# Kernel optimization log

Measured on AMD Instinct MI355X. Metric: run time of the kernel, lower is better.

The kernel has to match this reference:

```python
import jax, jax.numpy as jnp
from jax import lax
import numpy as np

HID = 64      # lstm hidden / gat in-dim
HEADS = 4
DH = HID // HEADS  # 16 per-head dim
OUT = 3       # horizon


def setup_inputs() -> dict:
    key = jax.random.key(0)
    ks = jax.random.split(key, 18)
    B, T, N = 8, 12, 1500
    p = lambda k, shape: jax.random.normal(k, shape, jnp.float32) * 0.1
    return {
        "x": jax.random.normal(ks[0], (B, T, N), jnp.float32),
        "adj": jax.random.randint(ks[1], (N, N), 0, 2, jnp.int32),
        "lstm_Wih0": p(ks[2], (4 * HID, 1)),
        "lstm_Whh0": p(ks[3], (4 * HID, HID)),
        "lstm_bih0": p(ks[4], (4 * HID,)),
        "lstm_bhh0": p(ks[5], (4 * HID,)),
        "lstm_Wih1": p(ks[6], (4 * HID, HID)),
        "lstm_Whh1": p(ks[7], (4 * HID, HID)),
        "lstm_bih1": p(ks[8], (4 * HID,)),
        "lstm_bhh1": p(ks[9], (4 * HID,)),
        "gat0_W": p(ks[10], (HID, HID)),
        "gat0_asrc": p(ks[11], (HEADS, DH)),
        "gat0_adst": p(ks[12], (HEADS, DH)),
        "gat1_W": p(ks[13], (HID, HID)),
        "gat1_asrc": p(ks[14], (HEADS, DH)),
        "gat1_adst": p(ks[15], (HEADS, DH)),
        "out_W": p(ks[16], (OUT, HID)),
        "out_b": p(ks[17], (OUT,)),
    }


def _lstm_layer(seq, Wih, Whh, bih, bhh):
    # seq: (T, BN, in) -> (T, BN, H). PyTorch gate order i,f,g,o.
    BN = seq.shape[1]
    H = Whh.shape[1]

    def step(carry, xt):
        h, c = carry
        g = xt @ Wih.T + h @ Whh.T + bih + bhh
        i, f, gg, o = jnp.split(g, 4, axis=-1)
        c = jax.nn.sigmoid(f) * c + jax.nn.sigmoid(i) * jnp.tanh(gg)
        h = jax.nn.sigmoid(o) * jnp.tanh(c)
        return (h, c), h

    zero = jnp.zeros((BN, H), seq.dtype)
    _, hs = lax.scan(step, (zero, zero), seq)
    return hs


def _gat(h_in, W, asrc, adst, mask):
    # h_in: (B,N,HID); mask: (1,N,N,1) bool
    B, N, _ = h_in.shape
    Hn, D = asrc.shape
    hp = (h_in @ W.T).reshape(B, N, Hn, D)           # (B,N,H,D)
    e_src = jnp.einsum('bnhd,hd->bnh', hp, asrc)
    e_dst = jnp.einsum('bnhd,hd->bnh', hp, adst)
    e = e_src[:, :, None, :] + e_dst[:, None, :, :]   # (B,i,j,H)
    e = jnp.where(e > 0, e, 0.2 * e)                  # LeakyReLU(0.2)
    e = jnp.where(mask, e, -jnp.inf)
    alpha = jax.nn.softmax(e, axis=2)                 # softmax over neighbors j
    ho = jnp.einsum('bijh,bjhd->bihd', alpha, hp)
    return ho.reshape(B, N, Hn * D)


def reference(x, adj, lstm_Wih0, lstm_Whh0, lstm_bih0, lstm_bhh0,
              lstm_Wih1, lstm_Whh1, lstm_bih1, lstm_bhh1,
              gat0_W, gat0_asrc, gat0_adst, gat1_W, gat1_asrc, gat1_adst,
              out_W, out_b):
    B, T, N = x.shape
    # (B,T,N) -> (B*N, T, 1) -> time-major (T, B*N, 1)
    xf = jnp.transpose(x, (0, 2, 1)).reshape(B * N, T, 1)
    seq = jnp.transpose(xf, (1, 0, 2))
    hs = _lstm_layer(seq, lstm_Wih0, lstm_Whh0, lstm_bih0, lstm_bhh0)
    hs = _lstm_layer(hs, lstm_Wih1, lstm_Whh1, lstm_bih1, lstm_bhh1)
    h = hs[-1].reshape(B, N, HID)                     # last-step hidden of top layer
    mask = (adj > 0)[None, :, :, None]
    h = jax.nn.relu(_gat(h, gat0_W, gat0_asrc, gat0_adst, mask))
    h = jax.nn.relu(_gat(h, gat1_W, gat1_asrc, gat1_adst, mask))
    out = h @ out_W.T + out_b                         # (B,N,OUT)
    return jnp.transpose(out, (0, 2, 1))              # (B,OUT,N)
```

## Files before the change

### kernel.cpp

```cpp
#include <hip/hip_runtime.h>
#include <hip/hip_bf16.h>


#define BN 12000
#define NNODE 1500
#define NB 8
#define TT 12
#define NPAD 1536
#define SEQB 48
#define LOG2E 1.44269504f

typedef __bf16 bf16x8 __attribute__((ext_vector_type(8)));
typedef __bf16 bf16x4 __attribute__((ext_vector_type(4)));
typedef float  f32x4  __attribute__((ext_vector_type(4)));

__device__ __forceinline__ float rcpf(float v) { return __builtin_amdgcn_rcpf(v); }
__device__ __forceinline__ float exp2f_(float v) { return __builtin_amdgcn_exp2f(v); }
__device__ __forceinline__ float sigf(float v) { return rcpf(1.f + __expf(-v)); }
__device__ __forceinline__ float tanhf_(float v) {
    return fmaf(2.f, rcpf(1.f + __expf(-2.f * v)), -1.f);
}

__global__ __launch_bounds__(256) void setup_kernel(
    const float* __restrict__ Whh0, const float* __restrict__ Wih1,
    const float* __restrict__ Whh1, const float* __restrict__ g0W,
    const float* __restrict__ g1W, const int* __restrict__ adj,
    __bf16* __restrict__ wb0, __bf16* __restrict__ wb1,
    __bf16* __restrict__ gw0, __bf16* __restrict__ gw1,
    unsigned int* __restrict__ mask)
{
    if (blockIdx.x < 224) {
        int i = blockIdx.x * 256 + threadIdx.x;
        if (i < 16384) {
            wb0[i] = (__bf16)Whh0[i];
        } else if (i < 49152) {
            int j = i - 16384;
            int g = j >> 7, k = j & 127;
            wb1[j] = (__bf16)(k < 64 ? Wih1[(g << 6) + k] : Whh1[(g << 6) + k - 64]);
        } else if (i < 53248) {
            gw0[i - 49152] = (__bf16)g0W[i - 49152];
        } else if (i < 57344) {
            gw1[i - 53248] = (__bf16)g1W[i - 53248];
        }
    } else {
        int idx  = (blockIdx.x - 224) * 4 + (threadIdx.x >> 6);
        int lane = threadIdx.x & 63;
        int i  = idx / 24;
        int ch = idx - i * 24;
        if (i >= 1504) return;
        int j = ch * 64 + lane;
        int a = (i < NNODE && j < NNODE) ? adj[i * NNODE + j] : 0;
        unsigned long long m = __ballot(a > 0);
        if (lane == 0) *(unsigned long long*)&mask[i * 48 + ch * 2] = m;
    }
}

__global__ __launch_bounds__(512, 1) void lstm_mfma(
    const float* __restrict__ x,
    const float* __restrict__ Wih0,
    const float* __restrict__ bih0, const float* __restrict__ bhh0,
    const float* __restrict__ bih1, const float* __restrict__ bhh1,
    const __bf16* __restrict__ wb0, const __bf16* __restrict__ wb1,
    float* __restrict__ hfin)
{
    __shared__ __align__(16) __bf16 h0s[SEQB * 72];
    __shared__ __align__(16) __bf16 h1s[SEQB * 72];
    __shared__ __align__(16) float  xls[TT * SEQB];

    int tid  = threadIdx.x;
    int w    = __builtin_amdgcn_readfirstlane(tid >> 6);
    int lane = tid & 63;
    int l15  = lane & 15;
    int qd   = lane >> 4;
    bool lo  = l15 < 8;
    int dloc = l15 & 7;
    int d    = 8 * w + dloc;

    for (int e = tid; e < (SEQB * 72) / 2; e += 512) ((unsigned int*)h1s)[e] = 0u;
    for (int e = tid; e < TT * SEQB; e += 512) {
        int t = e / SEQB, m = e - t * SEQB;
        int s = blockIdx.x * SEQB + m;
        int bb = s / NNODE, nn = s - bb * NNODE;
        xls[e] = x[bb * (TT * NNODE) + t * NNODE + nn];
    }

    int gA = (lo ? 0 : 64) + d;
    int gB = (lo ? 128 : 192) + d;
    bf16x8 B0A[2], B0B[2], B1A[4], B1B[4];
    #pragma unroll
    for (int kt = 0; kt < 2; ++kt) {
        B0A[kt] = *(const bf16x8*)&wb0[gA * 64 + 32 * kt + 8 * qd];
        B0B[kt] = *(const bf16x8*)&wb0[gB * 64 + 32 * kt + 8 * qd];
    }
    #pragma unroll
    for (int kt = 0; kt < 4; ++kt) {
        B1A[kt] = *(const bf16x8*)&wb1[gA * 128 + 32 * kt + 8 * qd];
        B1B[kt] = *(const bf16x8*)&wb1[gB * 128 + 32 * kt + 8 * qd];
    }
    float b0A = bih0[gA] + bhh0[gA], b0B = bih0[gB] + bhh0[gB];
    float b1A = bih1[gA] + bhh1[gA], b1B = bih1[gB] + bhh1[gB];
    float w0A = Wih0[gA], w0B = Wih0[gB];

    float pwi = Wih0[d],       pbi = bih0[d]       + bhh0[d];
    float pwg = Wih0[128 + d], pbg = bih0[128 + d] + bhh0[128 + d];
    float pwo = Wih0[192 + d], pbo = bih0[192 + d] + bhh0[192 + d];

    float c0[3][2], c1[3][2];
    #pragma unroll
    for (int mt = 0; mt < 3; ++mt) { c0[mt][0] = c0[mt][1] = c1[mt][0] = c1[mt][1] = 0.f; }

    __syncthreads();

    #pragma unroll
    for (int mt = 0; mt < 3; ++mt)
        #pragma unroll
        for (int rl = 0; rl < 2; ++rl) {
            int rr = lo ? rl : 2 + rl;
            int m = 16 * mt + 4 * qd + rr;
            float xv = xls[m];
            float gi = fmaf(pwi, xv, pbi);
            float gg = fmaf(pwg, xv, pbg);
            float go = fmaf(pwo, xv, pbo);
            float c = sigf(gi) * tanhf_(gg);
            c0[mt][rl] = c;
            h0s[m * 72 + d] = (__bf16)(sigf(go) * tanhf_(c));
        }
    __syncthreads();

    for (int t = 0; t < TT; ++t) {
        bool last = (t == TT - 1);
        bf16x8 a0[3][2], a1[3][2];
        #pragma unroll
        for (int mt = 0; mt < 3; ++mt)
            #pragma unroll
            for (int kt = 0; kt < 2; ++kt) {
                a0[mt][kt] = *(bf16x8*)&h0s[(16 * mt + l15) * 72 + 32 * kt + 8 * qd];
                a1[mt][kt] = *(bf16x8*)&h1s[(16 * mt + l15) * 72 + 32 * kt + 8 * qd];
            }
        f32x4 AA1[3], AB1[3], AA0[3], AB0[3];
        #pragma unroll
        for (int mt = 0; mt < 3; ++mt) {
            #pragma unroll
            for (int r = 0; r < 4; ++r) { AA1[mt][r] = b1A; AB1[mt][r] = b1B; }
            if (!last) {
                f32x4 xv = *(f32x4*)&xls[(t + 1) * SEQB + 16 * mt + 4 * qd];
                #pragma unroll
                for (int r = 0; r < 4; ++r) {
                    AA0[mt][r] = fmaf(w0A, xv[r], b0A);
                    AB0[mt][r] = fmaf(w0B, xv[r], b0B);
                }
            }
        }
        #pragma unroll
        for (int mt = 0; mt < 3; ++mt) {
            #pragma unroll
            for (int kt = 0; kt < 2; ++kt) {
                AA1[mt] = __builtin_amdgcn_mfma_f32_16x16x32_bf16(a0[mt][kt], B1A[kt], AA1[mt], 0, 0, 0);
                AB1[mt] = __builtin_amdgcn_mfma_f32_16x16x32_bf16(a0[mt][kt], B1B[kt], AB1[mt], 0, 0, 0);
                AA1[mt] = __builtin_amdgcn_mfma_f32_16x16x32_bf16(a1[mt][kt], B1A[kt + 2], AA1[mt], 0, 0, 0);
                AB1[mt] = __builtin_amdgcn_mfma_f32_16x16x32_bf16(a1[mt][kt], B1B[kt + 2], AB1[mt], 0, 0, 0);
            }
            if (!last) {
                #pragma unroll
                for (int kt = 0; kt < 2; ++kt) {
                    AA0[mt] = __builtin_amdgcn_mfma_f32_16x16x32_bf16(a0[mt][kt], B0A[kt], AA0[mt], 0, 0, 0);
                    AB0[mt] = __builtin_amdgcn_mfma_f32_16x16x32_bf16(a0[mt][kt], B0B[kt], AB0[mt], 0, 0, 0);
                }
            }
        }
        __syncthreads();

        #pragma unroll
        for (int mt = 0; mt < 3; ++mt) {
            {
                float shA0 = __shfl_xor(lo ? AA1[mt][2] : AA1[mt][0], 8);
                float shA1 = __shfl_xor(lo ? AA1[mt][3] : AA1[mt][1], 8);
                float shB0 = __shfl_xor(lo ? AB1[mt][2] : AB1[mt][0], 8);
                float shB1 = __shfl_xor(lo ? AB1[mt][3] : AB1[mt][1], 8);
                #pragma unroll
                for (int rl = 0; rl < 2; ++rl) {
                    int rr = lo ? rl : 2 + rl;
                    float ownA = AA1[mt][rr], ownB = AB1[mt][rr];
                    float shA = rl ? shA1 : shA0, shB = rl ? shB1 : shB0;
                    float gi = lo ? ownA : shA;
                    float gf = lo ? shA : ownA;
                    float gg = lo ? ownB : shB;
                    float go = lo ? shB : ownB;
                    float c = sigf(gf) * c1[mt][rl] + sigf(gi) * tanhf_(gg);
                    c1[mt][rl] = c;
                    float hv = sigf(go) * tanhf_(c);
                    int m = 16 * mt + 4 * qd + rr;
                    if (!last) h1s[m * 72 + d] = (__bf16)hv;
                    else       hfin[(blockIdx.x * SEQB + m) * 64 + d] = hv;
                }
            }
            if (!last) {
                float shA0 = __shfl_xor(lo ? AA0[mt][2] : AA0[mt][0], 8);
                float shA1 = __shfl_xor(lo ? AA0[mt][3] : AA0[mt][1], 8);
                float shB0 = __shfl_xor(lo ? AB0[mt][2] : AB0[mt][0], 8);
                float shB1 = __shfl_xor(lo ? AB0[mt][3] : AB0[mt][1], 8);
                #pragma unroll
                for (int rl = 0; rl < 2; ++rl) {
                    int rr = lo ? rl : 2 + rl;
                    float ownA = AA0[mt][rr], ownB = AB0[mt][rr];
                    float shA = rl ? shA1 : shA0, shB = rl ? shB1 : shB0;
                    float gi = lo ? ownA : shA;
                    float gf = lo ? shA : ownA;
                    float gg = lo ? ownB : shB;
                    float go = lo ? shB : ownB;
                    float c = sigf(gf) * c0[mt][rl] + sigf(gi) * tanhf_(gg);
                    c0[mt][rl] = c;
                    int m = 16 * mt + 4 * qd + rr;
                    h0s[m * 72 + d] = (__bf16)(sigf(go) * tanhf_(c));
                }
            }
        }
        __syncthreads();
    }
}

__global__ __launch_bounds__(256) void gat_prep(
    const float* __restrict__ hin, const __bf16* __restrict__ Wb,
    const float* __restrict__ asrc, const float* __restrict__ adst,
    __bf16* __restrict__ hpT, float* __restrict__ esT, float* __restrict__ edT)
{
    __shared__ __align__(16) __bf16 hp_t[64 * 72];
    __shared__ float avs[128];

    int tid  = threadIdx.x;
    int wv   = tid >> 6;
    int lane = tid & 63;
    int l15  = lane & 15;
    int qd   = lane >> 4;

    if (tid < 64)       avs[tid] = asrc[tid] * LOG2E;
    else if (tid < 128) avs[tid] = adst[tid - 64] * LOG2E;

    int s0 = blockIdx.x * 64;
    int sn = s0 + wv * 16 + l15;
    int snc = min(sn, BN - 1);

    bf16x8 Bf[2];
    #pragma unroll
    for (int kt = 0; kt < 2; ++kt) {
        f32x4 ha = *(const f32x4*)&hin[snc * 64 + kt * 32 + qd * 8];
        f32x4 hb = *(const f32x4*)&hin[snc * 64 + kt * 32 + qd * 8 + 4];
        bf16x8 bv;
        #pragma unroll
        for (int r = 0; r < 4; ++r) { bv[r] = (__bf16)ha[r]; bv[4 + r] = (__bf16)hb[r]; }
        Bf[kt] = bv;
    }
    __syncthreads();

    f32x4 acc[4];
    #pragma unroll
    for (int mt = 0; mt < 4; ++mt) {
        int dd = mt * 16 + l15;
        bf16x8 A0 = *(const bf16x8*)&Wb[dd * 64 + qd * 8];
        bf16x8 A1 = *(const bf16x8*)&Wb[dd * 64 + 32 + qd * 8];
        f32x4 a = {0.f, 0.f, 0.f, 0.f};
        a = __builtin_amdgcn_mfma_f32_16x16x32_bf16(A0, Bf[0], a, 0, 0, 0);
        a = __builtin_amdgcn_mfma_f32_16x16x32_bf16(A1, Bf[1], a, 0, 0, 0);
        acc[mt] = a;
    }

    #pragma unroll
    for (int mt = 0; mt < 4; ++mt) {
        float ts = 0.f, td = 0.f;
        #pragma unroll
        for (int r = 0; r < 4; ++r) {
            int dd = mt * 16 + qd * 4 + r;
            ts = fmaf(acc[mt][r], avs[dd], ts);
            td = fmaf(acc[mt][r], avs[64 + dd], td);
            hp_t[dd * 72 + wv * 16 + l15] = (__bf16)acc[mt][r];
        }
        ts += __shfl_xor(ts, 16); ts += __shfl_xor(ts, 32);
        td += __shfl_xor(td, 16); td += __shfl_xor(td, 32);
        if (qd == 0 && sn < BN) {
            int b = sn / NNODE, n = sn - b * NNODE;
            esT[(b * 4 + mt) * NPAD + n] = ts;
            edT[(b * 4 + mt) * NPAD + n] = td;
        }
    }
    __syncthreads();

    int dim = tid >> 2, seg = tid & 3;
    int b0 = s0 / NNODE, b1 = (s0 + 63) / NNODE;
    if (b0 == b1 && s0 + 63 < BN) {
        int n0 = s0 - b0 * NNODE;
        bf16x4 v0 = *(bf16x4*)&hp_t[dim * 72 + seg * 16];
        bf16x4 v1 = *(bf16x4*)&hp_t[dim * 72 + seg * 16 + 4];
        bf16x4 v2 = *(bf16x4*)&hp_t[dim * 72 + seg * 16 + 8];
        bf16x4 v3 = *(bf16x4*)&hp_t[dim * 72 + seg * 16 + 12];
        __bf16* dst = &hpT[((b0 << 6) + dim) * NPAD + n0 + seg * 16];
        *(bf16x4*)(dst)      = v0;
        *(bf16x4*)(dst + 4)  = v1;
        *(bf16x4*)(dst + 8)  = v2;
        *(bf16x4*)(dst + 12) = v3;
    } else {
        #pragma unroll
        for (int u = 0; u < 16; ++u) {
            int ss = s0 + seg * 16 + u;
            if (ss < BN) {
                int b = ss / NNODE, n = ss - b * NNODE;
                hpT[((b << 6) + dim) * NPAD + n] = hp_t[dim * 72 + seg * 16 + u];
            }
        }
    }
}

__global__ __launch_bounds__(512) void gat_agg(
    const __bf16* __restrict__ hpT, const float* __restrict__ esT,
    const float* __restrict__ edT, const unsigned int* __restrict__ mask,
    float* __restrict__ hout, const float* __restrict__ oW,
    const float* __restrict__ ob, float* __restrict__ outp, int final)
{
    __shared__ float Ss[8][16];
    __shared__ float hbuf[32 * 72];
    __shared__ float oWs[192];
    __shared__ float obs[3];

    int tid  = threadIdx.x;
    int wv   = tid >> 6;
    int lane = tid & 63;
    int l15  = lane & 15;
    int qd   = lane >> 4;
    int hh   = wv & 3;
    int ig   = wv >> 2;
    int b    = blockIdx.x / 47;
    int i0   = (blockIdx.x % 47) * 32;
    int it   = i0 + ig * 16;

    if (final) {
        if (tid < 192) oWs[tid] = oW[tid];
        if (tid < 3)   obs[tid] = ob[tid];
    }

    const __bf16* Brow = hpT + (((b << 6) + (hh << 4) + l15) * NPAD);
    const float* edrow = edT + (b * 4 + hh) * NPAD;
    const unsigned int* mrow = mask + (it + l15) * 48;
    float esv = esT[(b * 4 + hh) * NPAD + it + l15];

    f32x4 acc = {0.f, 0.f, 0.f, 0.f};
    float S = 0.f;

    for (int jt = 0; jt < 12; ++jt) {
        uint4 mw = *(const uint4*)&mrow[jt * 4];
        #pragma unroll
        for (int kt = 0; kt < 4; ++kt) {
            int jk = jt * 128 + kt * 32 + qd * 8;
            float4 e0 = *(const float4*)&edrow[jk];
            float4 e1 = *(const float4*)&edrow[jk + 4];
            unsigned int mb = ((&mw.x)[kt] >> (qd * 8)) & 0xffu;
            float ej[8] = {e0.x, e0.y, e0.z, e0.w, e1.x, e1.y, e1.z, e1.w};
            bf16x8 A;
            #pragma unroll
            for (int jj = 0; jj < 8; ++jj) {
                float e = esv + ej[jj];
                e = fmaxf(e, 0.2f * e);
                float p = ((mb >> jj) & 1u) ? exp2f_(e) : 0.f;
                S += p;
                A[jj] = (__bf16)p;
            }
            bf16x8 B = *(const bf16x8*)&Brow[jk];
            acc = __builtin_amdgcn_mfma_f32_16x16x32_bf16(A, B, acc, 0, 0, 0);
        }
    }

    S += __shfl_xor(S, 16);
    S += __shfl_xor(S, 32);
    if (qd == 0) Ss[wv][l15] = S;
    __syncthreads();

    if (!final) {
        #pragma unroll
        for (int r = 0; r < 4; ++r) {
            int i = it + qd * 4 + r;
            if (i < NNODE) {
                float rs = rcpf(Ss[wv][qd * 4 + r]);
                hout[((b * NNODE + i) << 6) + (hh << 4) + l15] = fmaxf(acc[r] * rs, 0.f);
            }
        }
    } else {
        #pragma unroll
        for (int r = 0; r < 4; ++r) {
            float rs = rcpf(Ss[wv][qd * 4 + r]);
            hbuf[(ig * 16 + qd * 4 + r) * 72 + (hh << 4) + l15] = fmaxf(acc[r] * rs, 0.f);
        }
        __syncthreads();
        if (tid < 384) {
            int idx = tid >> 2, ks = tid & 3;
            int nl = idx & 31, o = idx >> 5;
            if (i0 + nl < NNODE) {
                const float* hb = &hbuf[nl * 72 + ks * 16];
                float a = 0.f;
                #pragma unroll
                for (int kk = 0; kk < 16; ++kk)
                    a = fmaf(hb[kk], oWs[o * 64 + ks * 16 + kk], a);
                a += __shfl_xor(a, 1);
                a += __shfl_xor(a, 2);
                if (ks == 0)
                    outp[(long)b * 3 * NNODE + o * NNODE + i0 + nl] = a + obs[o];
            }
        }
    }
}

extern "C" void kernel_launch(void* const* d_in, const int* in_sizes, int n_in,
                              void* d_out, int out_size, void* d_ws, size_t ws_size,
                              hipStream_t stream) {
    const float* x    = (const float*)d_in[0];
    const int*   adj  = (const int*)d_in[1];
    const float* Wih0 = (const float*)d_in[2];
    const float* Whh0 = (const float*)d_in[3];
    const float* bih0 = (const float*)d_in[4];
    const float* bhh0 = (const float*)d_in[5];
    const float* Wih1 = (const float*)d_in[6];
    const float* Whh1 = (const float*)d_in[7];
    const float* bih1 = (const float*)d_in[8];
    const float* bhh1 = (const float*)d_in[9];
    const float* g0W  = (const float*)d_in[10];
    const float* g0s  = (const float*)d_in[11];
    const float* g0d  = (const float*)d_in[12];
    const float* g1W  = (const float*)d_in[13];
    const float* g1s  = (const float*)d_in[14];
    const float* g1d  = (const float*)d_in[15];
    const float* oW   = (const float*)d_in[16];
    const float* ob   = (const float*)d_in[17];

    float* ws = (float*)d_ws;
    float*        bufh  = ws;
    float*        esT   = ws + 768000;
    float*        edT   = ws + 817152;
    __bf16*       hpT   = (__bf16*)(ws + 866304);
    unsigned int* maskp = (unsigned int*)(ws + 1259520);
    __bf16*       wb0   = (__bf16*)(ws + 1331712);
    __bf16*       wb1   = (__bf16*)(ws + 1339904);
    __bf16*       gw0   = (__bf16*)(ws + 1356288);
    __bf16*       gw1   = (__bf16*)(ws + 1358336);

    setup_kernel<<<9248, 256, 0, stream>>>(Whh0, Wih1, Whh1, g0W, g1W, adj,
                                           wb0, wb1, gw0, gw1, maskp);
    lstm_mfma<<<250, 512, 0, stream>>>(x, Wih0, bih0, bhh0, bih1, bhh1,
                                       wb0, wb1, bufh);
    gat_prep<<<188, 256, 0, stream>>>(bufh, gw0, g0s, g0d, hpT, esT, edT);
    gat_agg<<<376, 512, 0, stream>>>(hpT, esT, edT, maskp, bufh,
                                     oW, ob, (float*)d_out, 0);
    gat_prep<<<188, 256, 0, stream>>>(bufh, gw1, g1s, g1d, hpT, esT, edT);
    gat_agg<<<376, 512, 0, stream>>>(hpT, esT, edT, maskp, bufh,
                                     oW, ob, (float*)d_out, 1);
}
```

Measured before the change: 231.6 us.

## Fuse setup into LSTM kernel, convert weights inline, shrink LSTM tile

Drops the separate setup kernel. Weights are now loaded as fp32 and converted to bf16 in registers inside the LSTM and GAT prep kernels, and the adjacency bitmask build runs in extra blocks of the same launch as the LSTM. Each LSTM block now handles 16 sequences instead of 48, giving 750 blocks instead of 250 so more CUs stay busy during the sequential time loop. The trade-offs are redundant weight loads and conversions in every block, and less MFMA work per block to hide latency.

```diff
diff --git a/kernel.cpp b/kernel.cpp
--- a/kernel.cpp
+++ b/kernel.cpp
@@ -7,7 +7,6 @@
 #define NB 8
 #define TT 12
 #define NPAD 1536
-#define SEQB 48
 #define LOG2E 1.44269504f
 
 typedef __bf16 bf16x8 __attribute__((ext_vector_type(8)));
@@ -21,51 +20,42 @@
     return fmaf(2.f, rcpf(1.f + __expf(-2.f * v)), -1.f);
 }
 
-__global__ __launch_bounds__(256) void setup_kernel(
-    const float* __restrict__ Whh0, const float* __restrict__ Wih1,
-    const float* __restrict__ Whh1, const float* __restrict__ g0W,
-    const float* __restrict__ g1W, const int* __restrict__ adj,
-    __bf16* __restrict__ wb0, __bf16* __restrict__ wb1,
-    __bf16* __restrict__ gw0, __bf16* __restrict__ gw1,
-    unsigned int* __restrict__ mask)
-{
-    if (blockIdx.x < 224) {
-        int i = blockIdx.x * 256 + threadIdx.x;
-        if (i < 16384) {
-            wb0[i] = (__bf16)Whh0[i];
-        } else if (i < 49152) {
-            int j = i - 16384;
-            int g = j >> 7, k = j & 127;
-            wb1[j] = (__bf16)(k < 64 ? Wih1[(g << 6) + k] : Whh1[(g << 6) + k - 64]);
-        } else if (i < 53248) {
-            gw0[i - 49152] = (__bf16)g0W[i - 49152];
-        } else if (i < 57344) {
-            gw1[i - 53248] = (__bf16)g1W[i - 53248];
-        }
-    } else {
-        int idx  = (blockIdx.x - 224) * 4 + (threadIdx.x >> 6);
-        int lane = threadIdx.x & 63;
-        int i  = idx / 24;
-        int ch = idx - i * 24;
-        if (i >= 1504) return;
-        int j = ch * 64 + lane;
-        int a = (i < NNODE && j < NNODE) ? adj[i * NNODE + j] : 0;
-        unsigned long long m = __ballot(a > 0);
-        if (lane == 0) *(unsigned long long*)&mask[i * 48 + ch * 2] = m;
-    }
-}
-
-__global__ __launch_bounds__(512, 1) void lstm_mfma(
+__device__ __forceinline__ bf16x8 ldcvt(const float* __restrict__ p) {
+    f32x4 a = *(const f32x4*)p;
+    f32x4 b = *(const f32x4*)(p + 4);
+    bf16x8 r;
+    #pragma unroll
+    for (int i = 0; i < 4; ++i) { r[i] = (__bf16)a[i]; r[4 + i] = (__bf16)b[i]; }
+    return r;
+}
+
+__global__ __launch_bounds__(512, 1) void lstm_mask(
     const float* __restrict__ x,
-    const float* __restrict__ Wih0,
+    const float* __restrict__ Wih0, const float* __restrict__ Whh0,
     const float* __restrict__ bih0, const float* __restrict__ bhh0,
+    const float* __restrict__ Wih1, const float* __restrict__ Whh1,
     const float* __restrict__ bih1, const float* __restrict__ bhh1,
-    const __bf16* __restrict__ wb0, const __bf16* __restrict__ wb1,
+    const int* __restrict__ adj, unsigned int* __restrict__ mask,
     float* __restrict__ hfin)
 {
-    __shared__ __align__(16) __bf16 h0s[SEQB * 72];
-    __shared__ __align__(16) __bf16 h1s[SEQB * 72];
-    __shared__ __align__(16) float  xls[TT * SEQB];
+    if (blockIdx.x >= 750) {
+        int wid  = (blockIdx.x - 750) * 8 + (threadIdx.x >> 6);
+        int lane = threadIdx.x & 63;
+        #pragma unroll 4
+        for (int u = 0; u < 16; ++u) {
+            int task = wid * 16 + u;
+            int i = task / 24, ch = task - i * 24;
+            int j = ch * 64 + lane;
+            int a = (i < NNODE && j < NNODE) ? adj[i * NNODE + j] : 0;
+            unsigned long long m = __ballot(a > 0);
+            if (lane == 0 && i < 1504) *(unsigned long long*)&mask[i * 48 + ch * 2] = m;
+        }
+        return;
+    }
+
+    __shared__ __align__(16) __bf16 h0s[16 * 72];
+    __shared__ __align__(16) __bf16 h1s[16 * 72];
+    __shared__ __align__(16) float  xls[TT * 16];
 
     int tid  = threadIdx.x;
     int w    = __builtin_amdgcn_readfirstlane(tid >> 6);
@@ -76,12 +66,12 @@
     int dloc = l15 & 7;
     int d    = 8 * w + dloc;
 
-    for (int e = tid; e < (SEQB * 72) / 2; e += 512) ((unsigned int*)h1s)[e] = 0u;
-    for (int e = tid; e < TT * SEQB; e += 512) {
-        int t = e / SEQB, m = e - t * SEQB;
-        int s = blockIdx.x * SEQB + m;
+    for (int e = tid; e < (16 * 72) / 2; e += 512) ((unsigned int*)h1s)[e] = 0u;
+    if (tid < TT * 16) {
+        int t = tid >> 4, m = tid & 15;
+        int s = blockIdx.x * 16 + m;
         int bb = s / NNODE, nn = s - bb * NNODE;
-        xls[e] = x[bb * (TT * NNODE) + t * NNODE + nn];
+        xls[tid] = x[bb * (TT * NNODE) + t * NNODE + nn];
     }
 
     int gA = (lo ? 0 : 64) + d;
@@ -89,13 +79,12 @@
     bf16x8 B0A[2], B0B[2], B1A[4], B1B[4];
     #pragma unroll
     for (int kt = 0; kt < 2; ++kt) {
-        B0A[kt] = *(const bf16x8*)&wb0[gA * 64 + 32 * kt + 8 * qd];
-        B0B[kt] = *(const bf16x8*)&wb0[gB * 64 + 32 * kt + 8 * qd];
-    }
-    #pragma unroll
-    for (int kt = 0; kt < 4; ++kt) {
-        B1A[kt] = *(const bf16x8*)&wb1[gA * 128 + 32 * kt + 8 * qd];
-        B1B[kt] = *(const bf16x8*)&wb1[gB * 128 + 32 * kt + 8 * qd];
+        B0A[kt] = ldcvt(&Whh0[gA * 64 + 32 * kt + 8 * qd]);
+        B0B[kt] = ldcvt(&Whh0[gB * 64 + 32 * kt + 8 * qd]);
+        B1A[kt] = ldcvt(&Wih1[gA * 64 + 32 * kt + 8 * qd]);
+        B1B[kt] = ldcvt(&Wih1[gB * 64 + 32 * kt + 8 * qd]);
+        B1A[kt + 2] = ldcvt(&Whh1[gA * 64 + 32 * kt + 8 * qd]);
+        B1B[kt + 2] = ldcvt(&Whh1[gB * 64 + 32 * kt + 8 * qd]);
     }
     float b0A = bih0[gA] + bhh0[gA], b0B = bih0[gB] + bhh0[gB];
     float b1A = bih1[gA] + bhh1[gA], b1B = bih1[gB] + bhh1[gB];
@@ -105,122 +94,108 @@
     float pwg = Wih0[128 + d], pbg = bih0[128 + d] + bhh0[128 + d];
     float pwo = Wih0[192 + d], pbo = bih0[192 + d] + bhh0[192 + d];
 
-    float c0[3][2], c1[3][2];
-    #pragma unroll
-    for (int mt = 0; mt < 3; ++mt) { c0[mt][0] = c0[mt][1] = c1[mt][0] = c1[mt][1] = 0.f; }
+    float c0[2], c1[2];
+    c0[0] = c0[1] = c1[0] = c1[1] = 0.f;
 
     __syncthreads();
 
     #pragma unroll
-    for (int mt = 0; mt < 3; ++mt)
-        #pragma unroll
-        for (int rl = 0; rl < 2; ++rl) {
-            int rr = lo ? rl : 2 + rl;
-            int m = 16 * mt + 4 * qd + rr;
-            float xv = xls[m];
-            float gi = fmaf(pwi, xv, pbi);
-            float gg = fmaf(pwg, xv, pbg);
-            float go = fmaf(pwo, xv, pbo);
-            float c = sigf(gi) * tanhf_(gg);
-            c0[mt][rl] = c;
-            h0s[m * 72 + d] = (__bf16)(sigf(go) * tanhf_(c));
-        }
+    for (int rl = 0; rl < 2; ++rl) {
+        int rr = lo ? rl : 2 + rl;
+        int m = 4 * qd + rr;
+        float xv = xls[m];
+        float gi = fmaf(pwi, xv, pbi);
+        float gg = fmaf(pwg, xv, pbg);
+        float go = fmaf(pwo, xv, pbo);
+        float c = sigf(gi) * tanhf_(gg);
+        c0[rl] = c;
+        h0s[m * 72 + d] = (__bf16)(sigf(go) * tanhf_(c));
+    }
     __syncthreads();
 
     for (int t = 0; t < TT; ++t) {
         bool last = (t == TT - 1);
-        bf16x8 a0[3][2], a1[3][2];
-        #pragma unroll
-        for (int mt = 0; mt < 3; ++mt)
+        bf16x8 a0[2], a1[2];
+        #pragma unroll
+        for (int kt = 0; kt < 2; ++kt) {
+            a0[kt] = *(bf16x8*)&h0s[l15 * 72 + 32 * kt + 8 * qd];
+            a1[kt] = *(bf16x8*)&h1s[l15 * 72 + 32 * kt + 8 * qd];
+        }
+        f32x4 AA1, AB1, AA0, AB0;
+        #pragma unroll
+        for (int r = 0; r < 4; ++r) { AA1[r] = b1A; AB1[r] = b1B; }
+        if (!last) {
+            f32x4 xv = *(f32x4*)&xls[(t + 1) * 16 + 4 * qd];
+            #pragma unroll
+            for (int r = 0; r < 4; ++r) {
+                AA0[r] = fmaf(w0A, xv[r], b0A);
+                AB0[r] = fmaf(w0B, xv[r], b0B);
+            }
+        }
+        #pragma unroll
+        for (int kt = 0; kt < 2; ++kt) {
+            AA1 = __builtin_amdgcn_mfma_f32_16x16x32_bf16(a0[kt], B1A[kt], AA1, 0, 0, 0);
+            AB1 = __builtin_amdgcn_mfma_f32_16x16x32_bf16(a0[kt], B1B[kt], AB1, 0, 0, 0);
+            AA1 = __builtin_amdgcn_mfma_f32_16x16x32_bf16(a1[kt], B1A[kt + 2], AA1, 0, 0, 0);
+            AB1 = __builtin_amdgcn_mfma_f32_16x16x32_bf16(a1[kt], B1B[kt + 2], AB1, 0, 0, 0);
+        }
+        if (!last) {
             #pragma unroll
             for (int kt = 0; kt < 2; ++kt) {
-                a0[mt][kt] = *(bf16x8*)&h0s[(16 * mt + l15) * 72 + 32 * kt + 8 * qd];
-                a1[mt][kt] = *(bf16x8*)&h1s[(16 * mt + l15) * 72 + 32 * kt + 8 * qd];
-            }
-        f32x4 AA1[3], AB1[3], AA0[3], AB0[3];
-        #pragma unroll
-        for (int mt = 0; mt < 3; ++mt) {
+                AA0 = __builtin_amdgcn_mfma_f32_16x16x32_bf16(a0[kt], B0A[kt], AA0, 0, 0, 0);
+                AB0 = __builtin_amdgcn_mfma_f32_16x16x32_bf16(a0[kt], B0B[kt], AB0, 0, 0, 0);
+            }
+        }
+        __syncthreads();
+
+        {
+            float shA0 = __shfl_xor(lo ? AA1[2] : AA1[0], 8);
+            float shA1 = __shfl_xor(lo ? AA1[3] : AA1[1], 8);
+            float shB0 = __shfl_xor(lo ? AB1[2] : AB1[0], 8);
+            float shB1 = __shfl_xor(lo ? AB1[3] : AB1[1], 8);
             #pragma unroll
-            for (int r = 0; r < 4; ++r) { AA1[mt][r] = b1A; AB1[mt][r] = b1B; }
-            if (!last) {
-                f32x4 xv = *(f32x4*)&xls[(t + 1) * SEQB + 16 * mt + 4 * qd];
-                #pragma unroll
-                for (int r = 0; r < 4; ++r) {
-                    AA0[mt][r] = fmaf(w0A, xv[r], b0A);
-                    AB0[mt][r] = fmaf(w0B, xv[r], b0B);
-                }
-            }
-        }
-        #pragma unroll
-        for (int mt = 0; mt < 3; ++mt) {
+            for (int rl = 0; rl < 2; ++rl) {
+                int rr = lo ? rl : 2 + rl;
+                float ownA = AA1[rr], ownB = AB1[rr];
+                float shA = rl ? shA1 : shA0, shB = rl ? shB1 : shB0;
+                float gi = lo ? ownA : shA;
+                float gf = lo ? shA : ownA;
+                float gg = lo ? ownB : shB;
+                float go = lo ? shB : ownB;
+                float c = sigf(gf) * c1[rl] + sigf(gi) * tanhf_(gg);
+                c1[rl] = c;
+                float hv = sigf(go) * tanhf_(c);
+                int m = 4 * qd + rr;
+                if (!last) h1s[m * 72 + d] = (__bf16)hv;
+                else       hfin[(blockIdx.x * 16 + m) * 64 + d] = hv;
+            }
+        }
+        if (!last) {
+            float shA0 = __shfl_xor(lo ? AA0[2] : AA0[0], 8);
+            float shA1 = __shfl_xor(lo ? AA0[3] : AA0[1], 8);
+            float shB0 = __shfl_xor(lo ? AB0[2] : AB0[0], 8);
+            float shB1 = __shfl_xor(lo ? AB0[3] : AB0[1], 8);
             #pragma unroll
-            for (int kt = 0; kt < 2; ++kt) {
-                AA1[mt] = __builtin_amdgcn_mfma_f32_16x16x32_bf16(a0[mt][kt], B1A[kt], AA1[mt], 0, 0, 0);
-                AB1[mt] = __builtin_amdgcn_mfma_f32_16x16x32_bf16(a0[mt][kt], B1B[kt], AB1[mt], 0, 0, 0);
-                AA1[mt] = __builtin_amdgcn_mfma_f32_16x16x32_bf16(a1[mt][kt], B1A[kt + 2], AA1[mt], 0, 0, 0);
-                AB1[mt] = __builtin_amdgcn_mfma_f32_16x16x32_bf16(a1[mt][kt], B1B[kt + 2], AB1[mt], 0, 0, 0);
-            }
-            if (!last) {
-                #pragma unroll
-                for (int kt = 0; kt < 2; ++kt) {
-                    AA0[mt] = __builtin_amdgcn_mfma_f32_16x16x32_bf16(a0[mt][kt], B0A[kt], AA0[mt], 0, 0, 0);
-                    AB0[mt] = __builtin_amdgcn_mfma_f32_16x16x32_bf16(a0[mt][kt], B0B[kt], AB0[mt], 0, 0, 0);
-                }
+            for (int rl = 0; rl < 2; ++rl) {
+                int rr = lo ? rl : 2 + rl;
+                float ownA = AA0[rr], ownB = AB0[rr];
+                float shA = rl ? shA1 : shA0, shB = rl ? shB1 : shB0;
+                float gi = lo ? ownA : shA;
+                float gf = lo ? shA : ownA;
+                float gg = lo ? ownB : shB;
+                float go = lo ? shB : ownB;
+                float c = sigf(gf) * c0[rl] + sigf(gi) * tanhf_(gg);
+                c0[rl] = c;
+                int m = 4 * qd + rr;
+                h0s[m * 72 + d] = (__bf16)(sigf(go) * tanhf_(c));
             }
         }
         __syncthreads();
-
-        #pragma unroll
-        for (int mt = 0; mt < 3; ++mt) {
-            {
-                float shA0 = __shfl_xor(lo ? AA1[mt][2] : AA1[mt][0], 8);
-                float shA1 = __shfl_xor(lo ? AA1[mt][3] : AA1[mt][1], 8);
-                float shB0 = __shfl_xor(lo ? AB1[mt][2] : AB1[mt][0], 8);
-                float shB1 = __shfl_xor(lo ? AB1[mt][3] : AB1[mt][1], 8);
-                #pragma unroll
-                for (int rl = 0; rl < 2; ++rl) {
-                    int rr = lo ? rl : 2 + rl;
-                    float ownA = AA1[mt][rr], ownB = AB1[mt][rr];
-                    float shA = rl ? shA1 : shA0, shB = rl ? shB1 : shB0;
-                    float gi = lo ? ownA : shA;
-                    float gf = lo ? shA : ownA;
-                    float gg = lo ? ownB : shB;
-                    float go = lo ? shB : ownB;
-                    float c = sigf(gf) * c1[mt][rl] + sigf(gi) * tanhf_(gg);
-                    c1[mt][rl] = c;
-                    float hv = sigf(go) * tanhf_(c);
-                    int m = 16 * mt + 4 * qd + rr;
-                    if (!last) h1s[m * 72 + d] = (__bf16)hv;
-                    else       hfin[(blockIdx.x * SEQB + m) * 64 + d] = hv;
-                }
-            }
-            if (!last) {
-                float shA0 = __shfl_xor(lo ? AA0[mt][2] : AA0[mt][0], 8);
-                float shA1 = __shfl_xor(lo ? AA0[mt][3] : AA0[mt][1], 8);
-                float shB0 = __shfl_xor(lo ? AB0[mt][2] : AB0[mt][0], 8);
-                float shB1 = __shfl_xor(lo ? AB0[mt][3] : AB0[mt][1], 8);
-                #pragma unroll
-                for (int rl = 0; rl < 2; ++rl) {
-                    int rr = lo ? rl : 2 + rl;
-                    float ownA = AA0[mt][rr], ownB = AB0[mt][rr];
-                    float shA = rl ? shA1 : shA0, shB = rl ? shB1 : shB0;
-                    float gi = lo ? ownA : shA;
-                    float gf = lo ? shA : ownA;
-                    float gg = lo ? ownB : shB;
-                    float go = lo ? shB : ownB;
-                    float c = sigf(gf) * c0[mt][rl] + sigf(gi) * tanhf_(gg);
-                    c0[mt][rl] = c;
-                    int m = 16 * mt + 4 * qd + rr;
-                    h0s[m * 72 + d] = (__bf16)(sigf(go) * tanhf_(c));
-                }
-            }
-        }
-        __syncthreads();
     }
 }
 
 __global__ __launch_bounds__(256) void gat_prep(
-    const float* __restrict__ hin, const __bf16* __restrict__ Wb,
+    const float* __restrict__ hin, const float* __restrict__ W,
     const float* __restrict__ asrc, const float* __restrict__ adst,
     __bf16* __restrict__ hpT, float* __restrict__ esT, float* __restrict__ edT)
 {
@@ -242,22 +217,15 @@
 
     bf16x8 Bf[2];
     #pragma unroll
-    for (int kt = 0; kt < 2; ++kt) {
-        f32x4 ha = *(const f32x4*)&hin[snc * 64 + kt * 32 + qd * 8];
-        f32x4 hb = *(const f32x4*)&hin[snc * 64 + kt * 32 + qd * 8 + 4];
-        bf16x8 bv;
-        #pragma unroll
-        for (int r = 0; r < 4; ++r) { bv[r] = (__bf16)ha[r]; bv[4 + r] = (__bf16)hb[r]; }
-        Bf[kt] = bv;
-    }
+    for (int kt = 0; kt < 2; ++kt) Bf[kt] = ldcvt(&hin[snc * 64 + kt * 32 + qd * 8]);
     __syncthreads();
 
     f32x4 acc[4];
     #pragma unroll
     for (int mt = 0; mt < 4; ++mt) {
         int dd = mt * 16 + l15;
-        bf16x8 A0 = *(const bf16x8*)&Wb[dd * 64 + qd * 8];
-        bf16x8 A1 = *(const bf16x8*)&Wb[dd * 64 + 32 + qd * 8];
+        bf16x8 A0 = ldcvt(&W[dd * 64 + qd * 8]);
+        bf16x8 A1 = ldcvt(&W[dd * 64 + 32 + qd * 8]);
         f32x4 a = {0.f, 0.f, 0.f, 0.f};
         a = __builtin_amdgcn_mfma_f32_16x16x32_bf16(A0, Bf[0], a, 0, 0, 0);
         a = __builtin_amdgcn_mfma_f32_16x16x32_bf16(A1, Bf[1], a, 0, 0, 0);
@@ -434,19 +402,14 @@
     float*        edT   = ws + 817152;
     __bf16*       hpT   = (__bf16*)(ws + 866304);
     unsigned int* maskp = (unsigned int*)(ws + 1259520);
-    __bf16*       wb0   = (__bf16*)(ws + 1331712);
-    __bf16*       wb1   = (__bf16*)(ws + 1339904);
-    __bf16*       gw0   = (__bf16*)(ws + 1356288);
-    __bf16*       gw1   = (__bf16*)(ws + 1358336);
-
-    setup_kernel<<<9248, 256, 0, stream>>>(Whh0, Wih1, Whh1, g0W, g1W, adj,
-                                           wb0, wb1, gw0, gw1, maskp);
-    lstm_mfma<<<250, 512, 0, stream>>>(x, Wih0, bih0, bhh0, bih1, bhh1,
-                                       wb0, wb1, bufh);
-    gat_prep<<<188, 256, 0, stream>>>(bufh, gw0, g0s, g0d, hpT, esT, edT);
+
+    lstm_mask<<<1032, 512, 0, stream>>>(x, Wih0, Whh0, bih0, bhh0,
+                                        Wih1, Whh1, bih1, bhh1,
+                                        adj, maskp, bufh);
+    gat_prep<<<188, 256, 0, stream>>>(bufh, g0W, g0s, g0d, hpT, esT, edT);
     gat_agg<<<376, 512, 0, stream>>>(hpT, esT, edT, maskp, bufh,
                                      oW, ob, (float*)d_out, 0);
-    gat_prep<<<188, 256, 0, stream>>>(bufh, gw1, g1s, g1d, hpT, esT, edT);
+    gat_prep<<<188, 256, 0, stream>>>(bufh, g1W, g1s, g1d, hpT, esT, edT);
     gat_agg<<<376, 512, 0, stream>>>(hpT, esT, edT, maskp, bufh,
                                      oW, ob, (float*)d_out, 1);
 }
```

New measurement: 231.8 us. No clear change (+0.1%).
